# Performance work log

Hardware: AMD Instinct MI355X
Metric: run time of the kernel (lower is better)

Reference implementation:

```python
import jax, jax.numpy as jnp
import numpy as np

N, S, EMB, H = 8, 1024, 512, 8
D = EMB // H  # head_dim = 64


def setup_inputs() -> dict:
    key = jax.random.key(0)
    ks = jax.random.split(key, 12)
    f = lambda k_, shp, s=1.0: jax.random.normal(k_, shp, dtype=jnp.float32) * s
    return {
        "v": f(ks[0], (N, S, EMB)),
        "k": f(ks[1], (N, S, EMB)),
        "q": f(ks[2], (N, S, EMB)),
        "Wv": f(ks[3], (D, D), 0.02), "bv": jnp.zeros((D,), jnp.float32),
        "Wk": f(ks[4], (D, D), 0.02), "bk": jnp.zeros((D,), jnp.float32),
        "Wq": f(ks[5], (D, D), 0.02), "bq": jnp.zeros((D,), jnp.float32),
        "E": f(ks[6], (1, S, D), 0.02),   # relative-position embedding
        "Wo": f(ks[7], (EMB, EMB), 0.02), "bo": jnp.zeros((EMB,), jnp.float32),
    }


def reference(v, k, q, Wv, bv, Wk, bk, Wq, bq, E, Wo, bo):
    n = v.shape[0]
    # per-head linear projections (module == 'spatiotemporal' branch)
    vals = v.reshape(n, S, H, D) @ Wv.T + bv   # (n,S,H,D)
    keys = k.reshape(n, S, H, D) @ Wk.T + bk
    qrs = q.reshape(n, S, H, D) @ Wq.T + bq

    # relative-position bias via skew trick (uses VALUES, as in source)
    QE = jnp.einsum('nlhd,sd->nhls', vals, E[0])            # (n,H,S,S)
    flip_mask = jnp.flip(jnp.triu(jnp.ones((S, S), bool), 1), axis=1)
    QE = jnp.where(flip_mask, 0.0, QE)                      # _mask_positions
    padded = jnp.pad(QE, ((0, 0), (0, 0), (0, 0), (1, 0)))  # left-pad last dim
    Sbias = padded.reshape(n, H, S + 1, S)[:, :, 1:, :]     # _skew -> (n,H,S,S)

    # attention scores with the source's mask semantics:
    # masked_fill(mask == 0, -1e20) keeps entries where triu(...,1) == 1
    qk = jnp.einsum('nqhd,nkhd->nhqk', qrs, keys)           # (n,H,S,S)
    keep = jnp.triu(jnp.ones((S, S), bool), 1)
    qk = jnp.where(keep, qk, jnp.float32(-1e20))

    attn = jax.nn.softmax(qk / jnp.sqrt(jnp.float32(EMB)), axis=3) + Sbias

    z = jnp.einsum('nhql,nlhd->nqhd', attn, vals).reshape(n, S, EMB)
    return z @ Wo.T + bo
```

## Files before the change

### kernel.cpp

```cpp
#include <hip/hip_runtime.h>
#include <hip/hip_bf16.h>

#define SDIM 1024
#define HNUM 8
#define DDIM 64
#define EMBD 512
#define NBATCH 8

static constexpr float SCALE = 0.044194173824159216f;

typedef short bf16x8 __attribute__((ext_vector_type(8)));
typedef float f32x4 __attribute__((ext_vector_type(4)));

__device__ __forceinline__ ushort bf16_of(float f) {
    return __builtin_bit_cast(unsigned short, __float2bfloat16(f));
}
__device__ __forceinline__ float f32_of(ushort u) {
    return __bfloat162float(__builtin_bit_cast(__hip_bfloat16, u));
}

__device__ __forceinline__ bf16x8 lds8(const ushort* base, int row, int slot) {
    return *(const bf16x8*)(base + (row * 8 + (slot ^ (row & 7))) * 8);
}

#define MFMA(a, b, c) __builtin_amdgcn_mfma_f32_16x16x32_bf16(a, b, c, 0, 0, 0)

__global__ __launch_bounds__(256) void proj_mfma(
    const float* __restrict__ xv, const float* __restrict__ xk, const float* __restrict__ xq,
    const float* __restrict__ Wv, const float* __restrict__ bv,
    const float* __restrict__ Wk, const float* __restrict__ bk,
    const float* __restrict__ Wq, const float* __restrict__ bq,
    ushort* __restrict__ vals_bf, ushort* __restrict__ keys_bf, ushort* __restrict__ qrs_bf,
    ushort* __restrict__ valsT_bf)
{
    __shared__ ushort a_s[256 * 64];
    __shared__ ushort w_s[64 * 64];

    const int blk = blockIdx.x;
    const int m = blk % 3;
    const int chunk = blk / 3;
    const int tok0 = chunk * 32;
    const int n = tok0 >> 10, s0 = tok0 & 1023;
    const int t = threadIdx.x;
    const int w = t >> 6, l = t & 63, lrow = l & 15, lgrp = l >> 4;

    const float* X = (m == 0) ? xv : (m == 1) ? xk : xq;
    const float* W = (m == 0) ? Wv : (m == 1) ? Wk : Wq;
    const float* B = (m == 0) ? bv : (m == 1) ? bk : bq;
    ushort* O = (m == 0) ? vals_bf : (m == 1) ? keys_bf : qrs_bf;

    #pragma unroll
    for (int i = 0; i < 16; ++i) {
        const int f4 = i * 256 + t;
        const int ls = f4 >> 7, c4 = f4 & 127;
        const int h = c4 >> 4, d4 = c4 & 15;
        const float4 v = ((const float4*)(X + (size_t)(tok0 + ls) * EMBD))[c4];
        ushort4 u;
        u.x = bf16_of(v.x); u.y = bf16_of(v.y); u.z = bf16_of(v.z); u.w = bf16_of(v.w);
        const int r = h * 32 + ls, slot = d4 >> 1;
        *(ushort4*)(a_s + (r * 8 + (slot ^ (r & 7))) * 8 + (d4 & 1) * 4) = u;
    }
    #pragma unroll
    for (int i = 0; i < 4; ++i) {
        const int f4 = i * 256 + t;
        const int r = f4 >> 4, d4 = f4 & 15;
        const float4 v = ((const float4*)W)[f4];
        ushort4 u;
        u.x = bf16_of(v.x); u.y = bf16_of(v.y); u.z = bf16_of(v.z); u.w = bf16_of(v.w);
        const int slot = d4 >> 1;
        *(ushort4*)(w_s + (r * 8 + (slot ^ (r & 7))) * 8 + (d4 & 1) * 4) = u;
    }
    __syncthreads();

    f32x4 acc[4][4];
    #pragma unroll
    for (int fr = 0; fr < 4; ++fr)
        #pragma unroll
        for (int fc = 0; fc < 4; ++fc) acc[fr][fc] = {0.f, 0.f, 0.f, 0.f};

    bf16x8 af[4][2];
    #pragma unroll
    for (int fr = 0; fr < 4; ++fr)
        #pragma unroll
        for (int kc = 0; kc < 2; ++kc)
            af[fr][kc] = lds8(a_s, w * 64 + fr * 16 + lrow, lgrp + kc * 4);

    #pragma unroll
    for (int fc = 0; fc < 4; ++fc)
        #pragma unroll
        for (int kc = 0; kc < 2; ++kc) {
            const bf16x8 bfr = lds8(w_s, fc * 16 + lrow, lgrp + kc * 4);
            #pragma unroll
            for (int fr = 0; fr < 4; ++fr)
                acc[fr][fc] = MFMA(af[fr][kc], bfr, acc[fr][fc]);
        }
    __syncthreads();

    float bias[4];
    #pragma unroll
    for (int fc = 0; fc < 4; ++fc) bias[fc] = B[fc * 16 + lrow];
    #pragma unroll
    for (int fr = 0; fr < 4; ++fr)
        #pragma unroll
        for (int fc = 0; fc < 4; ++fc)
            #pragma unroll
            for (int reg = 0; reg < 4; ++reg) {
                const int row = w * 64 + fr * 16 + lgrp * 4 + reg;
                const int col = fc * 16 + lrow;
                a_s[(row * 8 + ((col >> 3) ^ (row & 7))) * 8 + (col & 7)] =
                    bf16_of(acc[fr][fc][reg] + bias[fc]);
            }
    __syncthreads();

    #pragma unroll
    for (int i = 0; i < 8; ++i) {
        const int cc = i * 256 + t;
        const int r = cc >> 3, slot = cc & 7;
        const int h = r >> 5, ls = r & 31;
        const float4 v = *(const float4*)(a_s + (r * 8 + (slot ^ (r & 7))) * 8);
        *(float4*)(O + ((size_t)(n * HNUM + h) * SDIM + s0 + ls) * DDIM + slot * 8) = v;
    }

    if (m == 0) {
        #pragma unroll
        for (int i = 0; i < 2; ++i) {
            const int cid = i * 256 + t;
            const int hh = cid >> 6, d = cid & 63;
            union { ushort u[32]; float4 f[4]; } col;
            #pragma unroll
            for (int ls = 0; ls < 32; ++ls) {
                const int r = hh * 32 + ls;
                col.u[ls] = a_s[(r * 8 + ((d >> 3) ^ (r & 7))) * 8 + (d & 7)];
            }
            float4* dst = (float4*)(valsT_bf + ((size_t)(n * HNUM + hh) * DDIM + d) * SDIM + s0);
            dst[0] = col.f[0]; dst[1] = col.f[1]; dst[2] = col.f[2]; dst[3] = col.f[3];
        }
    }
}

__global__ __launch_bounds__(256) void conv_e(const float* __restrict__ E, ushort* __restrict__ e_bf) {
    const int i = blockIdx.x * 256 + threadIdx.x;
    e_bf[i] = bf16_of(E[i]);
}
__global__ __launch_bounds__(256) void conv_wo(const float* __restrict__ Wo, ushort* __restrict__ wo_bf) {
    const int i = blockIdx.x * 256 + threadIdx.x;
    wo_bf[i] = bf16_of(Wo[i]);
}

__global__ __launch_bounds__(512, 2) void attn_mfma(
    const ushort* __restrict__ vals_bf, const ushort* __restrict__ keys_bf,
    const ushort* __restrict__ qrs_bf, const ushort* __restrict__ valsT_bf,
    const ushort* __restrict__ e_bf, ushort* __restrict__ zh)
{
    __shared__ ushort k_s [64 * 64];
    __shared__ ushort vt_s[64 * 64];
    __shared__ ushort e_s [192 * 64];
    __shared__ ushort pe_s[128 * 64];
    __shared__ ushort pb_s[128 * 64];
    __shared__ float  vs_s[64];

    const int vid = blockIdx.x;
    const int blk = (vid & 7) * 64 + (vid >> 3);
    const int bt = blk & 7, h = (blk >> 3) & 7, n = blk >> 6;
    const int i0 = bt * 128;
    const int t = threadIdx.x;
    const int w = t >> 6, l = t & 63, lrow = l & 15, lgrp = l >> 4;
    const int s = w >> 2, q = w & 3;
    const int myit = 2 * bt + s;
    const int eoff = (1 - s) * 64;

    const ushort* Qb  = qrs_bf   + (n * HNUM + h) * (SDIM * DDIM);
    const ushort* Kb  = keys_bf  + (n * HNUM + h) * (SDIM * DDIM);
    const ushort* Vb  = vals_bf  + (n * HNUM + h) * (SDIM * DDIM);
    const ushort* VTb = valsT_bf + (n * HNUM + h) * (SDIM * DDIM);

    bf16x8 a_q[2], a_vi[2];
    {
        const int grow = i0 + w * 16 + lrow;
        #pragma unroll
        for (int kc = 0; kc < 2; ++kc) {
            a_q[kc]  = *(const bf16x8*)(Qb + grow * DDIM + kc * 32 + lgrp * 8);
            a_vi[kc] = *(const bf16x8*)(Vb + grow * DDIM + kc * 32 + lgrp * 8);
        }
    }
    if (t < 64) vs_s[t] = 0.f;

    f32x4 accn[4], accz[4];
    #pragma unroll
    for (int f = 0; f < 4; ++f) {
        accn[f] = {0.f, 0.f, 0.f, 0.f};
        accz[f] = {0.f, 0.f, 0.f, 0.f};
    }
    float den[4] = {0.f, 0.f, 0.f, 0.f};

    for (int jt = 0; jt < 16; ++jt) {
        const int j0 = jt * 64;
        const bool diag = (jt == myit);
        const bool needK = (jt >= 2 * bt);
        const bool needE = (jt <= 2 * bt + 1);
        __syncthreads();

        {
            const int row = t >> 3, slot = t & 7;
            const int sw = (row * 8 + (slot ^ (row & 7))) * 8;
            *(float4*)(vt_s + sw) = *(const float4*)(VTb + row * SDIM + j0 + slot * 8);
            if (needK)
                *(float4*)(k_s + sw) = *(const float4*)(Kb + (j0 + row) * DDIM + slot * 8);
        }
        if (needE) {
            const int ebU = SDIM - 128 - i0 + j0;
            #pragma unroll
            for (int i = 0; i < 3; ++i) {
                const int c = t + i * 512;
                const int row = c >> 3, slot = c & 7;
                const int g = ebU + row;
                float4 vv = make_float4(0.f, 0.f, 0.f, 0.f);
                if (g < SDIM) vv = *(const float4*)(e_bf + g * DDIM + slot * 8);
                *(float4*)(e_s + (row * 8 + (slot ^ (row & 7))) * 8) = vv;
            }
        }
        __syncthreads();

        if (bt == 7 && t < 64) {
            float sum = 0.f;
            #pragma unroll
            for (int slot = 0; slot < 8; ++slot) {
                const bf16x8 vv = lds8(vt_s, t, slot);
                #pragma unroll
                for (int u = 0; u < 8; ++u) sum += f32_of((ushort)vv[u]);
            }
            vs_s[t] += sum;
        }

        if (jt >= myit) {
            f32x4 sf[4];
            #pragma unroll
            for (int fc = 0; fc < 4; ++fc) sf[fc] = {0.f, 0.f, 0.f, 0.f};
            #pragma unroll
            for (int fc = 0; fc < 4; ++fc)
                if (!diag || fc >= q)
                    #pragma unroll
                    for (int kc = 0; kc < 2; ++kc)
                        sf[fc] = MFMA(a_q[kc], lds8(k_s, fc * 16 + lrow, lgrp + kc * 4), sf[fc]);
            #pragma unroll
            for (int fc = 0; fc < 4; ++fc) {
                #pragma unroll
                for (int r = 0; r < 4; ++r) {
                    const int rs = q * 16 + lgrp * 4 + r;
                    const int col = fc * 16 + lrow;
                    float e = 0.f;
                    if (!diag || col > rs) e = __expf(sf[fc][r] * SCALE);
                    den[r] += e;
                    const int prow = w * 16 + lgrp * 4 + r;
                    pe_s[(prow * 8 + ((col >> 3) ^ (prow & 7))) * 8 + (col & 7)] = bf16_of(e);
                }
            }
            bf16x8 ap[2];
            #pragma unroll
            for (int kc = 0; kc < 2; ++kc) ap[kc] = lds8(pe_s, w * 16 + lrow, lgrp + kc * 4);
            #pragma unroll
            for (int fc = 0; fc < 4; ++fc)
                #pragma unroll
                for (int kc = 0; kc < 2; ++kc)
                    accn[fc] = MFMA(ap[kc], lds8(vt_s, fc * 16 + lrow, lgrp + kc * 4), accn[fc]);
        }

        if (jt <= myit) {
            #pragma unroll
            for (int half = 0; half < 2; ++half) {
                f32x4 bd[4];
                #pragma unroll
                for (int fq = 0; fq < 4; ++fq) bd[fq] = {0.f, 0.f, 0.f, 0.f};
                #pragma unroll
                for (int fq = 0; fq < 4; ++fq) {
                    const int fc = half * 4 + fq;
                    const bool live = diag ? (fc <= 3 && fc + q >= 3)
                                           : (fc + q >= 3 && fc + q <= 7);
                    if (live)
                        #pragma unroll
                        for (int kc = 0; kc < 2; ++kc)
                            bd[fq] = MFMA(a_vi[kc], lds8(e_s, eoff + fc * 16 + lrow, lgrp + kc * 4), bd[fq]);
                }
                #pragma unroll
                for (int fq = 0; fq < 4; ++fq) {
                    const int fc = half * 4 + fq;
                    const bool touch = diag ? true : (fc + q >= 3 && fc + q <= 7);
                    if (touch) {
                        #pragma unroll
                        for (int r = 0; r < 4; ++r) {
                            const int rs = q * 16 + lgrp * 4 + r;
                            const int u = fc * 16 + lrow;
                            const int c = u - 63 + rs;
                            if (c >= 0 && c < 64) {
                                const float val = (diag && u > 63) ? 0.f : bd[fq][r];
                                const int prow = w * 16 + lgrp * 4 + r;
                                pb_s[(prow * 8 + ((c >> 3) ^ (prow & 7))) * 8 + (c & 7)] = bf16_of(val);
                            }
                        }
                    }
                }
            }
            bf16x8 ap[2];
            #pragma unroll
            for (int kc = 0; kc < 2; ++kc) ap[kc] = lds8(pb_s, w * 16 + lrow, lgrp + kc * 4);
            #pragma unroll
            for (int fc = 0; fc < 4; ++fc)
                #pragma unroll
                for (int kc = 0; kc < 2; ++kc)
                    accz[fc] = MFMA(ap[kc], lds8(vt_s, fc * 16 + lrow, lgrp + kc * 4), accz[fc]);
        }
    }

    __syncthreads();

    #pragma unroll
    for (int r = 0; r < 4; ++r) {
        float d = den[r];
        d += __shfl_xor(d, 1);
        d += __shfl_xor(d, 2);
        d += __shfl_xor(d, 4);
        d += __shfl_xor(d, 8);
        den[r] = d;
    }

    #pragma unroll
    for (int fc = 0; fc < 4; ++fc) {
        #pragma unroll
        for (int r = 0; r < 4; ++r) {
            const int grow = i0 + w * 16 + lgrp * 4 + r;
            const int col = fc * 16 + lrow;
            float o;
            if (grow == SDIM - 1)
                o = vs_s[col] * (1.0f / SDIM) + accz[fc][r];
            else
                o = accn[fc][r] / den[r] + accz[fc][r];
            zh[(size_t)(n * SDIM + grow) * EMBD + h * DDIM + col] = bf16_of(o);
        }
    }
}

__global__ __launch_bounds__(256) void out_mfma(
    const ushort* __restrict__ zh, const ushort* __restrict__ wo_bf,
    const float* __restrict__ bo, float* __restrict__ out)
{
    __shared__ ushort ah_s[128 * 64];
    __shared__ ushort b_s [64 * 64];

    const int vid = blockIdx.x;
    const int blk = (vid & 7) * 64 + (vid >> 3);
    const int r0 = (blk >> 3) * 128, c0 = (blk & 7) * 64;
    const int t = threadIdx.x;
    const int w = t >> 6, l = t & 63, lrow = l & 15, lgrp = l >> 4;

    f32x4 acc[2][4];
    #pragma unroll
    for (int fr = 0; fr < 2; ++fr)
        #pragma unroll
        for (int fc = 0; fc < 4; ++fc) acc[fr][fc] = {0.f, 0.f, 0.f, 0.f};

    for (int kt = 0; kt < 8; ++kt) {
        __syncthreads();
        #pragma unroll
        for (int i = 0; i < 4; ++i) {
            const int cc = i * 256 + t;
            const int r = cc >> 3, slot = cc & 7;
            const size_t src = (size_t)(r0 + r) * EMBD + kt * 64 + slot * 8;
            *(float4*)(ah_s + (r * 8 + (slot ^ (r & 7))) * 8) = *(const float4*)(zh + src);
        }
        #pragma unroll
        for (int i = 0; i < 2; ++i) {
            const int cc = i * 256 + t;
            const int r = cc >> 3, slot = cc & 7;
            const float4 vb = *(const float4*)(wo_bf + (size_t)(c0 + r) * EMBD + kt * 64 + slot * 8);
            *(float4*)(b_s + (r * 8 + (slot ^ (r & 7))) * 8) = vb;
        }
        __syncthreads();

        #pragma unroll
        for (int kc = 0; kc < 2; ++kc)
            #pragma unroll
            for (int fc = 0; fc < 4; ++fc) {
                const bf16x8 bfr = lds8(b_s, fc * 16 + lrow, lgrp + kc * 4);
                #pragma unroll
                for (int fr = 0; fr < 2; ++fr)
                    acc[fr][fc] = MFMA(lds8(ah_s, w * 32 + fr * 16 + lrow, lgrp + kc * 4), bfr, acc[fr][fc]);
            }
    }

    float bias[4];
    #pragma unroll
    for (int fc = 0; fc < 4; ++fc) bias[fc] = bo[c0 + fc * 16 + lrow];
    #pragma unroll
    for (int fr = 0; fr < 2; ++fr)
        #pragma unroll
        for (int fc = 0; fc < 4; ++fc)
            #pragma unroll
            for (int reg = 0; reg < 4; ++reg) {
                const int row = r0 + w * 32 + fr * 16 + lgrp * 4 + reg;
                const int col = c0 + fc * 16 + lrow;
                out[(size_t)row * EMBD + col] = acc[fr][fc][reg] + bias[fc];
            }
}

extern "C" void kernel_launch(void* const* d_in, const int* in_sizes, int n_in,
                              void* d_out, int out_size, void* d_ws, size_t ws_size,
                              hipStream_t stream) {
    const float* v  = (const float*)d_in[0];
    const float* k  = (const float*)d_in[1];
    const float* q  = (const float*)d_in[2];
    const float* Wv = (const float*)d_in[3];
    const float* bv = (const float*)d_in[4];
    const float* Wk = (const float*)d_in[5];
    const float* bk = (const float*)d_in[6];
    const float* Wq = (const float*)d_in[7];
    const float* bq = (const float*)d_in[8];
    const float* E  = (const float*)d_in[9];
    const float* Wo = (const float*)d_in[10];
    const float* bo = (const float*)d_in[11];
    float* out = (float*)d_out;

    char* ws = (char*)d_ws;
    ushort* qrs_bf   = (ushort*)(ws);
    ushort* keys_bf  = (ushort*)(ws + ((size_t)8 << 20));
    ushort* vals_bf  = (ushort*)(ws + ((size_t)16 << 20));
    ushort* valsT_bf = (ushort*)(ws + ((size_t)24 << 20));
    ushort* e_bf     = (ushort*)(ws + ((size_t)32 << 20));
    ushort* wo_bf    = (ushort*)(ws + ((size_t)33 << 20));
    ushort* zh       = (ushort*)(ws + ((size_t)34 << 20));

    proj_mfma<<<768, 256, 0, stream>>>(v, k, q, Wv, bv, Wk, bk, Wq, bq,
                                       vals_bf, keys_bf, qrs_bf, valsT_bf);
    conv_e<<<(SDIM * DDIM) / 256, 256, 0, stream>>>(E, e_bf);
    conv_wo<<<(EMBD * EMBD) / 256, 256, 0, stream>>>(Wo, wo_bf);
    attn_mfma<<<512, 512, 0, stream>>>(vals_bf, keys_bf, qrs_bf,
                                       valsT_bf, e_bf, zh);
    out_mfma<<<512, 256, 0, stream>>>(zh, wo_bf, bo, out);
}
```

Before: 113.5 us.

## Prefetch next tile of VT, K and E into registers during compute

Global loads for the next 64-wide tile of transposed values, keys and relative-position embeddings are now issued right after the barrier, into registers, and written to shared memory at the start of the next iteration. This overlaps global-memory latency with the MFMA work of the current tile instead of stalling on loads before each barrier. The cost is about 20 extra VGPRs per thread held across the loop, which could reduce occupancy.

Result: slower. 119.0 us (+4.8%).

```diff
diff --git a/kernel.cpp b/kernel.cpp
--- a/kernel.cpp
+++ b/kernel.cpp
@@ -193,6 +193,27 @@
     }
     float den[4] = {0.f, 0.f, 0.f, 0.f};
 
+    const int srow = t >> 3, sslot = t & 7;
+    const int sw = (srow * 8 + (sslot ^ (srow & 7))) * 8;
+
+    float4 r_vt, r_k, r_e0, r_e1, r_e2;
+
+    {
+        r_vt = *(const float4*)(VTb + srow * SDIM + sslot * 8);
+        if (bt == 0)
+            r_k = *(const float4*)(Kb + srow * DDIM + sslot * 8);
+        {
+            const int ebU = SDIM - 128 - i0;
+            const float4 z4 = make_float4(0.f, 0.f, 0.f, 0.f);
+            int g = ebU + srow;
+            r_e0 = (g < SDIM) ? *(const float4*)(e_bf + g * DDIM + sslot * 8) : z4;
+            g += 64;
+            r_e1 = (g < SDIM) ? *(const float4*)(e_bf + g * DDIM + sslot * 8) : z4;
+            g += 64;
+            r_e2 = (g < SDIM) ? *(const float4*)(e_bf + g * DDIM + sslot * 8) : z4;
+        }
+    }
+
     for (int jt = 0; jt < 16; ++jt) {
         const int j0 = jt * 64;
         const bool diag = (jt == myit);
@@ -201,25 +222,33 @@
         __syncthreads();
 
         {
-            const int row = t >> 3, slot = t & 7;
-            const int sw = (row * 8 + (slot ^ (row & 7))) * 8;
-            *(float4*)(vt_s + sw) = *(const float4*)(VTb + row * SDIM + j0 + slot * 8);
+            *(float4*)(vt_s + sw) = r_vt;
             if (needK)
-                *(float4*)(k_s + sw) = *(const float4*)(Kb + (j0 + row) * DDIM + slot * 8);
-        }
-        if (needE) {
-            const int ebU = SDIM - 128 - i0 + j0;
-            #pragma unroll
-            for (int i = 0; i < 3; ++i) {
-                const int c = t + i * 512;
-                const int row = c >> 3, slot = c & 7;
-                const int g = ebU + row;
-                float4 vv = make_float4(0.f, 0.f, 0.f, 0.f);
-                if (g < SDIM) vv = *(const float4*)(e_bf + g * DDIM + slot * 8);
-                *(float4*)(e_s + (row * 8 + (slot ^ (row & 7))) * 8) = vv;
+                *(float4*)(k_s + sw) = r_k;
+            if (needE) {
+                *(float4*)(e_s + sw)            = r_e0;
+                *(float4*)(e_s + sw + 64 * 64)  = r_e1;
+                *(float4*)(e_s + sw + 128 * 64) = r_e2;
             }
         }
         __syncthreads();
+
+        if (jt < 15) {
+            const int j1 = j0 + 64;
+            r_vt = *(const float4*)(VTb + srow * SDIM + j1 + sslot * 8);
+            if (jt + 1 >= 2 * bt)
+                r_k = *(const float4*)(Kb + (j1 + srow) * DDIM + sslot * 8);
+            if (jt + 1 <= 2 * bt + 1) {
+                const int ebU = SDIM - 128 - i0 + j1;
+                const float4 z4 = make_float4(0.f, 0.f, 0.f, 0.f);
+                int g = ebU + srow;
+                r_e0 = (g < SDIM) ? *(const float4*)(e_bf + g * DDIM + sslot * 8) : z4;
+                g += 64;
+                r_e1 = (g < SDIM) ? *(const float4*)(e_bf + g * DDIM + sslot * 8) : z4;
+                g += 64;
+                r_e2 = (g < SDIM) ? *(const float4*)(e_bf + g * DDIM + sslot * 8) : z4;
+            }
+        }
 
         if (bt == 7 && t < 64) {
             float sum = 0.f;
```
